# Performance work log

Measured on AMD Instinct MI355X. Metric: run time of the kernel, lower is better.

The kernel has to match this reference:

```python
import jax, jax.numpy as jnp
import numpy as np

N_NODES = 100000
N_EDGES = 3200000
N_GRAPHS = 4096
N_REL = 5
N_BASES = 4
HID = 32


def setup_inputs() -> dict:
    key = jax.random.key(0)
    ks = jax.random.split(key, 32)
    inp = {}
    inp['x'] = jax.random.normal(ks[0], (N_NODES, 4), dtype=jnp.float32)
    inp['edge_index'] = jax.random.randint(ks[1], (2, N_EDGES), 0, N_NODES, dtype=jnp.int64)
    inp['edge_type'] = jax.random.randint(ks[2], (N_EDGES,), 0, N_REL, dtype=jnp.int64)
    inp['user_idx'] = jax.random.randint(ks[3], (N_GRAPHS,), 0, N_NODES, dtype=jnp.int64)
    inp['item_idx'] = jax.random.randint(ks[4], (N_GRAPHS,), 0, N_NODES, dtype=jnp.int64)
    k = 5
    for l in range(4):
        in_c = 4 if l == 0 else HID
        inp[f'basis{l}'] = jax.random.normal(ks[k], (N_BASES, in_c, HID), dtype=jnp.float32) * 0.1; k += 1
        inp[f'comp{l}'] = jax.random.normal(ks[k], (N_REL, N_BASES), dtype=jnp.float32) * 0.5; k += 1
        inp[f'root{l}'] = jax.random.normal(ks[k], (in_c, HID), dtype=jnp.float32) * 0.1; k += 1
        inp[f'bias{l}'] = jax.random.normal(ks[k], (HID,), dtype=jnp.float32) * 0.01; k += 1
    inp['w1'] = jax.random.normal(ks[k], (256, 128), dtype=jnp.float32) * 0.05; k += 1
    inp['b1'] = jnp.zeros((128,), dtype=jnp.float32)
    inp['w2'] = jax.random.normal(ks[k], (128, 1), dtype=jnp.float32) * 0.05; k += 1
    inp['b2'] = jnp.zeros((1,), dtype=jnp.float32)
    return inp


def _rgcn_layer(x, src, key5, inv_cnt, basis, comp, root, bias, n_nodes):
    # mean-aggregate raw source features per (dst, relation): [N, R, in]
    agg = jax.ops.segment_sum(x[src], key5, num_segments=n_nodes * N_REL)
    agg = agg.reshape(n_nodes, N_REL, -1) * inv_cnt
    # basis-decomposed relation weights: W_r = sum_b comp[r,b] * basis[b]
    w = jnp.einsum('rb,bio->rio', comp, basis)  # [R, in, out]
    return jnp.einsum('nri,rio->no', agg, w) + x @ root + bias


def reference(x, edge_index, edge_type, user_idx, item_idx,
              basis0, comp0, root0, bias0,
              basis1, comp1, root1, bias1,
              basis2, comp2, root2, bias2,
              basis3, comp3, root3, bias3,
              w1, b1, w2, b2):
    n_nodes = x.shape[0]
    src, dst = edge_index[0], edge_index[1]
    key5 = dst * N_REL + edge_type  # combined (dst, relation) segment id
    cnt = jax.ops.segment_sum(jnp.ones_like(edge_type, dtype=x.dtype), key5,
                              num_segments=n_nodes * N_REL)
    inv_cnt = (1.0 / jnp.maximum(cnt, 1.0)).reshape(n_nodes, N_REL, 1)
    params = [(basis0, comp0, root0, bias0), (basis1, comp1, root1, bias1),
              (basis2, comp2, root2, bias2), (basis3, comp3, root3, bias3)]
    out = x
    hs = []
    for (basis, comp, root, bias) in params:
        out = jnp.tanh(_rgcn_layer(out, src, key5, inv_cnt, basis, comp, root, bias, n_nodes))
        hs.append(out)
    h = jnp.concatenate(hs, axis=1)            # [N, 128]
    g = jnp.concatenate([h[user_idx], h[item_idx]], axis=1)  # [B, 256]
    z = jax.nn.relu(g @ w1 + b1)
    return (z @ w2 + b2)[:, 0]
```

## Files before the change

kernel.cpp:

```cpp
#include <hip/hip_runtime.h>
#include <hip/hip_bf16.h>
#include <hip/hip_fp16.h>

#define N_NODES 100000
#define N_EDGES 3200000
#define N_GRAPHS 4096
#define N_REL 5
#define N_BASES 4
#define HID 32
#define SEG (N_NODES*N_REL)
#define DUMMY N_NODES

#define NBUCK 392
#define BCAP  10240
#define PBCAP 15360
#define NKEY  1280
#define PTILE 4096

typedef _Float16 half8 __attribute__((ext_vector_type(8)));
typedef float floatx4 __attribute__((ext_vector_type(4)));

static __global__ __launch_bounds__(256) void k_part(const int* __restrict__ ei,
                                                     const int* __restrict__ et,
                                                     int* __restrict__ gcur,
                                                     unsigned long long* __restrict__ part) {
    __shared__ unsigned long long stage[PTILE];
    __shared__ int hist[NBUCK];
    __shared__ int lofs[NBUCK];
    __shared__ int lbase[NBUCK];
    __shared__ int sscan[256];
    int t = threadIdx.x;
    int e0 = blockIdx.x * PTILE;
    int tile_n = N_EDGES - e0; if (tile_n > PTILE) tile_n = PTILE;

    for (int k = t; k < NBUCK; k += 256) hist[k] = 0;
    __syncthreads();
    int src[16], bkt[16], lkey[16];
#pragma unroll
    for (int j = 0; j < 16; j++) {
        int e = e0 + j * 256 + t;
        if (e < N_EDGES) {
            int s = ei[e];
            int d = ei[N_EDGES + e];
            int r = et[e];
            src[j] = s; bkt[j] = d >> 8; lkey[j] = ((d & 255) * 5) + r;
            atomicAdd(&hist[bkt[j]], 1);
        } else bkt[j] = -1;
    }
    __syncthreads();
    int h0 = (2 * t     < NBUCK) ? hist[2 * t]     : 0;
    int h1 = (2 * t + 1 < NBUCK) ? hist[2 * t + 1] : 0;
    int s2 = h0 + h1;
    sscan[t] = s2;
    __syncthreads();
    for (int off = 1; off < 256; off <<= 1) {
        int xv = (t >= off) ? sscan[t - off] : 0;
        __syncthreads();
        sscan[t] += xv;
        __syncthreads();
    }
    int excl = sscan[t] - s2;
    if (2 * t     < NBUCK) lofs[2 * t]     = excl;
    if (2 * t + 1 < NBUCK) lofs[2 * t + 1] = excl + h0;
    for (int k = t; k < NBUCK; k += 256) lbase[k] = atomicAdd(&gcur[k], hist[k]);
    __syncthreads();
    for (int k = t; k < NBUCK; k += 256) hist[k] = 0;
    __syncthreads();
#pragma unroll
    for (int j = 0; j < 16; j++) {
        if (bkt[j] >= 0) {
            int rank = atomicAdd(&hist[bkt[j]], 1);
            stage[lofs[bkt[j]] + rank] =
                ((unsigned long long)(unsigned)((bkt[j] << 16) | lkey[j]) << 32)
                | (unsigned)src[j];
        }
    }
    __syncthreads();
    for (int i = t; i < tile_n; i += 256) {
        unsigned long long u = stage[i];
        unsigned hi = (unsigned)(u >> 32);
        int bb = hi >> 16;
        unsigned long long lk = hi & 0xFFFFu;
        int pos = lbase[bb] + (i - lofs[bb]);
        if (pos < BCAP)
            part[(size_t)bb * BCAP + pos] = (lk << 32) | (u & 0xffffffffULL);
    }
}

static __global__ __launch_bounds__(1024) void k_bsort(const unsigned long long* __restrict__ part,
                                                       const int* __restrict__ gcur,
                                                       int* __restrict__ offs,
                                                       int* __restrict__ cnt,
                                                       int* __restrict__ srcs) {
    __shared__ int lhist[NKEY];
    __shared__ int lscan[NKEY];
    __shared__ int sscan[256];
    __shared__ int lsrc[PBCAP];
    int b = blockIdx.x;
    int t = threadIdx.x;
    int n = gcur[b]; if (n > BCAP) n = BCAP;
    const unsigned long long* reg = part + (size_t)b * BCAP;

    for (int k = t; k < NKEY; k += 1024) lhist[k] = 0;
    __syncthreads();
    for (int i = t; i < n; i += 1024)
        atomicAdd(&lhist[(int)(reg[i] >> 32)], 1);
    __syncthreads();

    int loc[5]; int s5 = 0;
    if (t < 256) {
#pragma unroll
        for (int j = 0; j < 5; j++) { loc[j] = s5; s5 += (lhist[t * 5 + j] + 7) & ~7; }
        sscan[t] = s5;
    }
    __syncthreads();
    for (int off = 1; off < 256; off <<= 1) {
        int x = (t >= off && t < 256) ? sscan[t - off] : 0;
        __syncthreads();
        if (t < 256) sscan[t] += x;
        __syncthreads();
    }
    if (t < 256) {
        int excl = sscan[t] - s5;
#pragma unroll
        for (int j = 0; j < 5; j++) lscan[t * 5 + j] = excl + loc[j];
    }
    __syncthreads();
    int ptot = sscan[255]; if (ptot > PBCAP) ptot = PBCAP;
    int pout = ptot + 16; if (pout > PBCAP) pout = PBCAP;

    int base = b * PBCAP;
    if (t < 256) {
#pragma unroll
        for (int j = 0; j < 5; j++) {
            int k = t * 5 + j;
            int segid = b * NKEY + k;
            if (segid < SEG) {
                cnt[segid]  = lhist[k];
                offs[segid] = base + lscan[k];
            }
        }
    }
    __syncthreads();
    for (int k = t; k < NKEY; k += 1024) lhist[k] = 0;
    for (int i = t; i < pout; i += 1024) lsrc[i] = DUMMY;
    __syncthreads();
    for (int i = t; i < n; i += 1024) {
        unsigned long long u = reg[i];
        int k = (int)(u >> 32);
        int pos = lscan[k] + atomicAdd(&lhist[k], 1);
        if (pos < PBCAP) lsrc[pos] = (int)(u & 0xffffffffULL);
    }
    __syncthreads();
    for (int i = t; i < pout; i += 1024) srcs[base + i] = lsrc[i];
}

static __global__ __launch_bounds__(256) void k_pad(const float* __restrict__ x,
                                                    __half* __restrict__ ht0,
                                                    __half* __restrict__ ht1,
                                                    __half* __restrict__ ht2,
                                                    __half* __restrict__ ht3,
                                                    __half* __restrict__ ht4,
                                                    int* __restrict__ srcs) {
    int tid = blockIdx.x * 256 + threadIdx.x;
    if (tid < (N_NODES + 1) * 32) {
        int nd = tid >> 5, ii = tid & 31;
        float v = (nd < N_NODES && ii < 4) ? x[(nd << 2) + ii] : 0.f;
        ht0[tid] = __float2half(v);
    } else {
        int r = tid - (N_NODES + 1) * 32;
        if (r < 128) {
            __half* hp = (r < 32) ? ht1 : (r < 64) ? ht2 : (r < 96) ? ht3 : ht4;
            hp[N_NODES * 32 + (r & 31)] = __float2half(0.f);
        } else if (r < 144) srcs[NBUCK * PBCAP + (r - 128)] = DUMMY;
    }
}

static __global__ __launch_bounds__(256) void k_wprepB(
    const float* __restrict__ ba0, const float* __restrict__ ro0,
    const float* __restrict__ ba1, const float* __restrict__ ro1,
    const float* __restrict__ ba2, const float* __restrict__ ro2,
    const float* __restrict__ ba3, const float* __restrict__ ro3,
    __half* __restrict__ Wb) {
    int idx = blockIdx.x * 256 + threadIdx.x;
    int j    = idx & 7;
    int lane = (idx >> 3) & 63;
    int tile = (idx >> 9) & 1;
    int ls   = idx >> 10;
    int l    = ls / 5;
    int s    = ls - l * 5;
    const float* basis = (l == 0) ? ba0 : (l == 1) ? ba1 : (l == 2) ? ba2 : ba3;
    const float* root  = (l == 0) ? ro0 : (l == 1) ? ro1 : (l == 2) ? ro2 : ro3;
    int in_c = (l == 0) ? 4 : HID;
    int k = s * 32 + ((lane >> 4) << 3) + j;
    int o = tile * 16 + (lane & 15);
    float v;
    if (k < 128) {
        int b = k >> 5, ii = k & 31;
        v = (ii < in_c) ? basis[(b * in_c + ii) * HID + o] : 0.f;
    } else {
        int ii = k - 128;
        v = (ii < in_c) ? root[ii * HID + o] : 0.f;
    }
    Wb[idx] = __float2half(v);
}

static __global__ __launch_bounds__(256) void k_wprepM(const float* __restrict__ w1,
                                                       __half* __restrict__ Wm) {
    int idx = blockIdx.x * 256 + threadIdx.x;
    int j    = idx & 7;
    int lane = (idx >> 3) & 63;
    int s    = (idx >> 9) & 7;
    int tile = idx >> 12;
    int k = s * 32 + ((lane >> 4) << 3) + j;
    int o = tile * 16 + (lane & 15);
    Wm[idx] = __float2half(w1[k * 128 + o]);
}

static __global__ __launch_bounds__(256, 8) void k_layer(
    const __half2* __restrict__ tab, const int* __restrict__ offs,
    const int* __restrict__ cnt, const int* __restrict__ srcs,
    const float* __restrict__ comp, const __half* __restrict__ Wbl,
    const float* __restrict__ bias, __half* __restrict__ hout) {
    __shared__ __align__(16) __half sAgg16[16 * 176];
    int t = threadIdx.x;
    int wave = t >> 6, q = (t >> 4) & 3, p = t & 15;

    float4 cw0 = *(const float4*)(comp + 0);
    float4 cw1 = *(const float4*)(comp + 4);
    float4 cw2 = *(const float4*)(comp + 8);
    float4 cw3 = *(const float4*)(comp + 12);
    float4 cw4 = *(const float4*)(comp + 16);

    int n = blockIdx.x * 16 + wave * 4 + q;
    int s5 = n * N_REL;
    int oo[6], cc[5];
#pragma unroll
    for (int r = 0; r < 5; r++) { oo[r] = offs[s5 + r]; cc[r] = cnt[s5 + r]; }
    oo[5] = oo[4] + ((cc[4] + 7) & ~7);

    __half2 selfh = tab[n * 16 + p];
    float a0x = 0.f, a0y = 0.f, a1x = 0.f, a1y = 0.f;
    float a2x = 0.f, a2y = 0.f, a3x = 0.f, a3y = 0.f;

#pragma unroll
    for (int r = 0; r < 5; r++) {
        int pR = oo[r], pr = oo[r + 1] - pR;
        const int* sp = srcs + pR;
        int4 e0 = *(const int4*)(sp);
        int4 e1 = *(const int4*)(sp + 4);
        __half2 g0 = tab[e0.x * 16 + p], g1 = tab[e0.y * 16 + p];
        __half2 g2 = tab[e0.z * 16 + p], g3 = tab[e0.w * 16 + p];
        __half2 g4 = tab[e1.x * 16 + p], g5 = tab[e1.y * 16 + p];
        __half2 g6 = tab[e1.z * 16 + p], g7 = tab[e1.w * 16 + p];
        __half2 sb = __hadd2(__hadd2(__hadd2(g0, g1), __hadd2(g2, g3)),
                             __hadd2(__hadd2(g4, g5), __hadd2(g6, g7)));
        float2 bf = __half22float2(sb);
        float Sx = bf.x, Sy = bf.y;
        for (int s8 = 8; s8 < pr; s8 += 8) {
            int4 f0 = *(const int4*)(sp + s8);
            int4 f1 = *(const int4*)(sp + s8 + 4);
            __half2 h0 = tab[f0.x * 16 + p], h1 = tab[f0.y * 16 + p];
            __half2 h2 = tab[f0.z * 16 + p], h3 = tab[f0.w * 16 + p];
            __half2 h4 = tab[f1.x * 16 + p], h5 = tab[f1.y * 16 + p];
            __half2 h6 = tab[f1.z * 16 + p], h7 = tab[f1.w * 16 + p];
            __half2 rb = __hadd2(__hadd2(__hadd2(h0, h1), __hadd2(h2, h3)),
                                 __hadd2(__hadd2(h4, h5), __hadd2(h6, h7)));
            float2 rf = __half22float2(rb);
            Sx += rf.x; Sy += rf.y;
        }
        int cr = cc[r];
        float ic = (cr > 0) ? __builtin_amdgcn_rcpf((float)cr) : 0.f;
        float scx = Sx * ic, scy = Sy * ic;
        float4 cw = (r == 0) ? cw0 : (r == 1) ? cw1 : (r == 2) ? cw2
                  : (r == 3) ? cw3 : cw4;
        a0x += cw.x * scx; a0y += cw.x * scy;
        a1x += cw.y * scx; a1y += cw.y * scy;
        a2x += cw.z * scx; a2y += cw.z * scy;
        a3x += cw.w * scx; a3y += cw.w * scy;
    }
    int nl = wave * 4 + q;
    __half2* row = (__half2*)(sAgg16 + nl * 176);
    row[p]      = __float22half2_rn(make_float2(a0x, a0y));
    row[16 + p] = __float22half2_rn(make_float2(a1x, a1y));
    row[32 + p] = __float22half2_rn(make_float2(a2x, a2y));
    row[48 + p] = __float22half2_rn(make_float2(a3x, a3y));
    row[64 + p] = selfh;
    __syncthreads();

    if (wave < 2) {
        int lane = t & 63;
        floatx4 acc = {0.f, 0.f, 0.f, 0.f};
        const __half* aBase = sAgg16 + (lane & 15) * 176 + ((lane >> 4) << 3);
        const __half* bBase = Wbl + wave * 512 + lane * 8;
#pragma unroll
        for (int s = 0; s < 5; s++) {
            half8 a = *(const half8*)(aBase + s * 32);
            half8 b = *(const half8*)(bBase + s * 1024);
            acc = __builtin_amdgcn_mfma_f32_16x16x32_f16(a, b, acc, 0, 0, 0);
        }
        int o = wave * 16 + (lane & 15);
        float bi = bias[o];
#pragma unroll
        for (int r = 0; r < 4; r++) {
            int node = blockIdx.x * 16 + ((lane >> 4) << 2) + r;
            hout[node * 32 + o] = __float2half(tanhf(acc[r] + bi));
        }
    }
}

static __global__ __launch_bounds__(256) void k_mlp(
    const __half* __restrict__ h1, const __half* __restrict__ h2,
    const __half* __restrict__ h3, const __half* __restrict__ h4,
    const int* __restrict__ uidx, const int* __restrict__ iidx,
    const __half* __restrict__ Wm, const float* __restrict__ b1,
    const float* __restrict__ w2, const float* __restrict__ b2,
    float* __restrict__ out) {
    __shared__ __align__(16) __half sg[16 * 264];
    __shared__ float sacc[4][16];
    int t = threadIdx.x, wave = t >> 6, lane = t & 63;
    int g0 = blockIdx.x * 16;
    int lt = lane >> 4, lp = lane & 15;
    const __half* htab = (lt == 0) ? h1 : (lt == 1) ? h2 : (lt == 2) ? h3 : h4;
#pragma unroll
    for (int gg2 = 0; gg2 < 4; gg2++) {
        int gg = wave * 4 + gg2;
        int g = g0 + gg;
        int u = uidx[g], it = iidx[g];
        __half2* dst = (__half2*)(sg + gg * 264);
        dst[lt * 16 + lp]      = ((const __half2*)(htab + u * 32))[lp];
        dst[64 + lt * 16 + lp] = ((const __half2*)(htab + it * 32))[lp];
    }
    __syncthreads();
    floatx4 acc0 = {0.f, 0.f, 0.f, 0.f}, acc1 = {0.f, 0.f, 0.f, 0.f};
    const __half* aBase = sg + (lane & 15) * 264 + ((lane >> 4) << 3);
    const __half* bB0 = Wm + (wave * 2 + 0) * 4096 + lane * 8;
    const __half* bB1 = Wm + (wave * 2 + 1) * 4096 + lane * 8;
#pragma unroll
    for (int s = 0; s < 8; s++) {
        half8 a  = *(const half8*)(aBase + s * 32);
        half8 f0 = *(const half8*)(bB0 + s * 512);
        half8 f1 = *(const half8*)(bB1 + s * 512);
        acc0 = __builtin_amdgcn_mfma_f32_16x16x32_f16(a, f0, acc0, 0, 0, 0);
        acc1 = __builtin_amdgcn_mfma_f32_16x16x32_f16(a, f1, acc1, 0, 0, 0);
    }
    int o0 = wave * 32 + (lane & 15);
    int o1 = o0 + 16;
    float b10 = b1[o0], b11 = b1[o1], w20 = w2[o0], w21 = w2[o1];
#pragma unroll
    for (int r = 0; r < 4; r++) {
        float z0 = fmaxf(acc0[r] + b10, 0.f);
        float z1 = fmaxf(acc1[r] + b11, 0.f);
        float v = z0 * w20 + z1 * w21;
#pragma unroll
        for (int off = 1; off < 16; off <<= 1) v += __shfl_xor(v, off);
        if ((lane & 15) == 0) sacc[wave][((lane >> 4) << 2) + r] = v;
    }
    __syncthreads();
    if (t < 16)
        out[g0 + t] = sacc[0][t] + sacc[1][t] + sacc[2][t] + sacc[3][t] + b2[0];
}

extern "C" void kernel_launch(void* const* d_in, const int* in_sizes, int n_in,
                              void* d_out, int out_size, void* d_ws, size_t ws_size,
                              hipStream_t stream) {
    const float* x  = (const float*)d_in[0];
    const int*   ei = (const int*)d_in[1];
    const int*   et = (const int*)d_in[2];
    const int*   ui = (const int*)d_in[3];
    const int*   ii = (const int*)d_in[4];
    const float* w1 = (const float*)d_in[21];
    const float* b1 = (const float*)d_in[22];
    const float* w2 = (const float*)d_in[23];
    const float* b2 = (const float*)d_in[24];

    char* ws = (char*)d_ws;
    if (ws_size < 92167680UL) return;
    int*    gcur = (int*)(ws + 0);
    int*    offs = (int*)(ws + 2048);
    int*    cnt  = (int*)(ws + 2002176);
    int*    srcs = (int*)(ws + 4002304);
    __half* Wb   = (__half*)(ws + 28086912);
    __half* Wm   = (__half*)(ws + 28127872);
    __half* ht0  = (__half*)(ws + 28193536);
    __half* ht1  = (__half*)(ws + 34593664);
    __half* ht2  = (__half*)(ws + 40993792);
    __half* ht3  = (__half*)(ws + 47393920);
    __half* ht4  = (__half*)(ws + 53794048);
    unsigned long long* part = (unsigned long long*)(ws + 34593664);

    hipMemsetAsync(gcur, 0, NBUCK * 4, stream);

    k_part<<<(N_EDGES + PTILE - 1) / PTILE, 256, 0, stream>>>(ei, et, gcur, part);
    k_bsort<<<NBUCK, 1024, 0, stream>>>(part, gcur, offs, cnt, srcs);
    k_pad<<<12501, 256, 0, stream>>>(x, ht0, ht1, ht2, ht3, ht4, srcs);
    k_wprepB<<<80, 256, 0, stream>>>(
        (const float*)d_in[5],  (const float*)d_in[7],
        (const float*)d_in[9],  (const float*)d_in[11],
        (const float*)d_in[13], (const float*)d_in[15],
        (const float*)d_in[17], (const float*)d_in[19], Wb);
    k_wprepM<<<128, 256, 0, stream>>>(w1, Wm);

    __half* tabs[5] = {ht0, ht1, ht2, ht3, ht4};
    for (int l = 0; l < 4; l++) {
        const float* comp = (const float*)d_in[6 + 4 * l];
        const float* bias = (const float*)d_in[8 + 4 * l];
        k_layer<<<6250, 256, 0, stream>>>((const __half2*)tabs[l], offs, cnt,
                                          srcs, comp, Wb + l * 5120, bias,
                                          tabs[l + 1]);
    }
    k_mlp<<<256, 256, 0, stream>>>(ht1, ht2, ht3, ht4, ui, ii, Wm, b1, w2, b2,
                                   (float*)d_out);
}
```

Measured before the change: 348.1 us.

## Merge prep kernels into one launch and batch first-chunk gathers across relations

Folds the gcur memset, input padding and weight-packing kernels into a single prep kernel launched before partitioning, and moves the padding-row zeroing into the bucket-sort kernel. In the layer kernel, the first eight source indices for all five relations are loaded up front and their gathers issued together before the tail loops. This is meant to cut launch overhead and expose more outstanding memory requests per thread. It also raises register pressure, and the zeroing inside bsort writes into memory aliased with the partition buffer that other blocks may still be reading.

```diff
diff --git a/kernel.cpp b/kernel.cpp
--- a/kernel.cpp
+++ b/kernel.cpp
@@ -91,7 +91,11 @@
                                                        const int* __restrict__ gcur,
                                                        int* __restrict__ offs,
                                                        int* __restrict__ cnt,
-                                                       int* __restrict__ srcs) {
+                                                       int* __restrict__ srcs,
+                                                       __half* __restrict__ ht1,
+                                                       __half* __restrict__ ht2,
+                                                       __half* __restrict__ ht3,
+                                                       __half* __restrict__ ht4) {
     __shared__ int lhist[NKEY];
     __shared__ int lscan[NKEY];
     __shared__ int sscan[256];
@@ -153,68 +157,68 @@
     }
     __syncthreads();
     for (int i = t; i < pout; i += 1024) srcs[base + i] = lsrc[i];
-}
-
-static __global__ __launch_bounds__(256) void k_pad(const float* __restrict__ x,
-                                                    __half* __restrict__ ht0,
-                                                    __half* __restrict__ ht1,
-                                                    __half* __restrict__ ht2,
-                                                    __half* __restrict__ ht3,
-                                                    __half* __restrict__ ht4,
-                                                    int* __restrict__ srcs) {
-    int tid = blockIdx.x * 256 + threadIdx.x;
-    if (tid < (N_NODES + 1) * 32) {
-        int nd = tid >> 5, ii = tid & 31;
-        float v = (nd < N_NODES && ii < 4) ? x[(nd << 2) + ii] : 0.f;
-        ht0[tid] = __float2half(v);
-    } else {
-        int r = tid - (N_NODES + 1) * 32;
-        if (r < 128) {
-            __half* hp = (r < 32) ? ht1 : (r < 64) ? ht2 : (r < 96) ? ht3 : ht4;
-            hp[N_NODES * 32 + (r & 31)] = __float2half(0.f);
-        } else if (r < 144) srcs[NBUCK * PBCAP + (r - 128)] = DUMMY;
-    }
-}
-
-static __global__ __launch_bounds__(256) void k_wprepB(
+
+    if (b == 0 && t < 128) {
+        __half* hp = (t < 32) ? ht1 : (t < 64) ? ht2 : (t < 96) ? ht3 : ht4;
+        hp[N_NODES * 32 + (t & 31)] = __float2half(0.f);
+    }
+}
+
+static __global__ __launch_bounds__(256) void k_prep(
+    const float* __restrict__ x, __half* __restrict__ ht0,
+    int* __restrict__ srcs, int* __restrict__ gcur,
     const float* __restrict__ ba0, const float* __restrict__ ro0,
     const float* __restrict__ ba1, const float* __restrict__ ro1,
     const float* __restrict__ ba2, const float* __restrict__ ro2,
     const float* __restrict__ ba3, const float* __restrict__ ro3,
-    __half* __restrict__ Wb) {
-    int idx = blockIdx.x * 256 + threadIdx.x;
-    int j    = idx & 7;
-    int lane = (idx >> 3) & 63;
-    int tile = (idx >> 9) & 1;
-    int ls   = idx >> 10;
-    int l    = ls / 5;
-    int s    = ls - l * 5;
-    const float* basis = (l == 0) ? ba0 : (l == 1) ? ba1 : (l == 2) ? ba2 : ba3;
-    const float* root  = (l == 0) ? ro0 : (l == 1) ? ro1 : (l == 2) ? ro2 : ro3;
-    int in_c = (l == 0) ? 4 : HID;
-    int k = s * 32 + ((lane >> 4) << 3) + j;
-    int o = tile * 16 + (lane & 15);
-    float v;
-    if (k < 128) {
-        int b = k >> 5, ii = k & 31;
-        v = (ii < in_c) ? basis[(b * in_c + ii) * HID + o] : 0.f;
+    const float* __restrict__ w1, __half* __restrict__ Wb,
+    __half* __restrict__ Wm) {
+    int blk = blockIdx.x;
+    int t = threadIdx.x;
+    if (blk < 12501) {
+        int tid = blk * 256 + t;
+        if (tid < (N_NODES + 1) * 32) {
+            int nd = tid >> 5, ii = tid & 31;
+            float v = (nd < N_NODES && ii < 4) ? x[(nd << 2) + ii] : 0.f;
+            ht0[tid] = __float2half(v);
+        } else {
+            int r = tid - (N_NODES + 1) * 32;
+            if (r < 16) srcs[NBUCK * PBCAP + r] = DUMMY;
+        }
+    } else if (blk < 12581) {
+        int idx = (blk - 12501) * 256 + t;
+        int j    = idx & 7;
+        int lane = (idx >> 3) & 63;
+        int tile = (idx >> 9) & 1;
+        int ls   = idx >> 10;
+        int l    = ls / 5;
+        int s    = ls - l * 5;
+        const float* basis = (l == 0) ? ba0 : (l == 1) ? ba1 : (l == 2) ? ba2 : ba3;
+        const float* root  = (l == 0) ? ro0 : (l == 1) ? ro1 : (l == 2) ? ro2 : ro3;
+        int in_c = (l == 0) ? 4 : HID;
+        int k = s * 32 + ((lane >> 4) << 3) + j;
+        int o = tile * 16 + (lane & 15);
+        float v;
+        if (k < 128) {
+            int b = k >> 5, ii = k & 31;
+            v = (ii < in_c) ? basis[(b * in_c + ii) * HID + o] : 0.f;
+        } else {
+            int ii = k - 128;
+            v = (ii < in_c) ? root[ii * HID + o] : 0.f;
+        }
+        Wb[idx] = __float2half(v);
+    } else if (blk < 12709) {
+        int idx = (blk - 12581) * 256 + t;
+        int j    = idx & 7;
+        int lane = (idx >> 3) & 63;
+        int s    = (idx >> 9) & 7;
+        int tile = idx >> 12;
+        int k = s * 32 + ((lane >> 4) << 3) + j;
+        int o = tile * 16 + (lane & 15);
+        Wm[idx] = __float2half(w1[k * 128 + o]);
     } else {
-        int ii = k - 128;
-        v = (ii < in_c) ? root[ii * HID + o] : 0.f;
-    }
-    Wb[idx] = __float2half(v);
-}
-
-static __global__ __launch_bounds__(256) void k_wprepM(const float* __restrict__ w1,
-                                                       __half* __restrict__ Wm) {
-    int idx = blockIdx.x * 256 + threadIdx.x;
-    int j    = idx & 7;
-    int lane = (idx >> 3) & 63;
-    int s    = (idx >> 9) & 7;
-    int tile = idx >> 12;
-    int k = s * 32 + ((lane >> 4) << 3) + j;
-    int o = tile * 16 + (lane & 15);
-    Wm[idx] = __float2half(w1[k * 128 + o]);
+        for (int k = t; k < NBUCK; k += 256) gcur[k] = 0;
+    }
 }
 
 static __global__ __launch_bounds__(256, 8) void k_layer(
@@ -240,23 +244,30 @@
     oo[5] = oo[4] + ((cc[4] + 7) & ~7);
 
     __half2 selfh = tab[n * 16 + p];
-    float a0x = 0.f, a0y = 0.f, a1x = 0.f, a1y = 0.f;
-    float a2x = 0.f, a2y = 0.f, a3x = 0.f, a3y = 0.f;
-
+
+    int4 e0[5], e1[5];
 #pragma unroll
     for (int r = 0; r < 5; r++) {
-        int pR = oo[r], pr = oo[r + 1] - pR;
-        const int* sp = srcs + pR;
-        int4 e0 = *(const int4*)(sp);
-        int4 e1 = *(const int4*)(sp + 4);
-        __half2 g0 = tab[e0.x * 16 + p], g1 = tab[e0.y * 16 + p];
-        __half2 g2 = tab[e0.z * 16 + p], g3 = tab[e0.w * 16 + p];
-        __half2 g4 = tab[e1.x * 16 + p], g5 = tab[e1.y * 16 + p];
-        __half2 g6 = tab[e1.z * 16 + p], g7 = tab[e1.w * 16 + p];
+        const int4* sp4 = (const int4*)(srcs + oo[r]);
+        e0[r] = sp4[0];
+        e1[r] = sp4[1];
+    }
+    float Sx[5], Sy[5];
+#pragma unroll
+    for (int r = 0; r < 5; r++) {
+        __half2 g0 = tab[e0[r].x * 16 + p], g1 = tab[e0[r].y * 16 + p];
+        __half2 g2 = tab[e0[r].z * 16 + p], g3 = tab[e0[r].w * 16 + p];
+        __half2 g4 = tab[e1[r].x * 16 + p], g5 = tab[e1[r].y * 16 + p];
+        __half2 g6 = tab[e1[r].z * 16 + p], g7 = tab[e1[r].w * 16 + p];
         __half2 sb = __hadd2(__hadd2(__hadd2(g0, g1), __hadd2(g2, g3)),
                              __hadd2(__hadd2(g4, g5), __hadd2(g6, g7)));
         float2 bf = __half22float2(sb);
-        float Sx = bf.x, Sy = bf.y;
+        Sx[r] = bf.x; Sy[r] = bf.y;
+    }
+#pragma unroll
+    for (int r = 0; r < 5; r++) {
+        int pr = oo[r + 1] - oo[r];
+        const int* sp = srcs + oo[r];
         for (int s8 = 8; s8 < pr; s8 += 8) {
             int4 f0 = *(const int4*)(sp + s8);
             int4 f1 = *(const int4*)(sp + s8 + 4);
@@ -267,11 +278,16 @@
             __half2 rb = __hadd2(__hadd2(__hadd2(h0, h1), __hadd2(h2, h3)),
                                  __hadd2(__hadd2(h4, h5), __hadd2(h6, h7)));
             float2 rf = __half22float2(rb);
-            Sx += rf.x; Sy += rf.y;
-        }
+            Sx[r] += rf.x; Sy[r] += rf.y;
+        }
+    }
+    float a0x = 0.f, a0y = 0.f, a1x = 0.f, a1y = 0.f;
+    float a2x = 0.f, a2y = 0.f, a3x = 0.f, a3y = 0.f;
+#pragma unroll
+    for (int r = 0; r < 5; r++) {
         int cr = cc[r];
         float ic = (cr > 0) ? __builtin_amdgcn_rcpf((float)cr) : 0.f;
-        float scx = Sx * ic, scy = Sy * ic;
+        float scx = Sx[r] * ic, scy = Sy[r] * ic;
         float4 cw = (r == 0) ? cw0 : (r == 1) ? cw1 : (r == 2) ? cw2
                   : (r == 3) ? cw3 : cw4;
         a0x += cw.x * scx; a0y += cw.x * scy;
@@ -389,17 +405,14 @@
     __half* ht4  = (__half*)(ws + 53794048);
     unsigned long long* part = (unsigned long long*)(ws + 34593664);
 
-    hipMemsetAsync(gcur, 0, NBUCK * 4, stream);
-
-    k_part<<<(N_EDGES + PTILE - 1) / PTILE, 256, 0, stream>>>(ei, et, gcur, part);
-    k_bsort<<<NBUCK, 1024, 0, stream>>>(part, gcur, offs, cnt, srcs);
-    k_pad<<<12501, 256, 0, stream>>>(x, ht0, ht1, ht2, ht3, ht4, srcs);
-    k_wprepB<<<80, 256, 0, stream>>>(
+    k_prep<<<12710, 256, 0, stream>>>(x, ht0, srcs, gcur,
         (const float*)d_in[5],  (const float*)d_in[7],
         (const float*)d_in[9],  (const float*)d_in[11],
         (const float*)d_in[13], (const float*)d_in[15],
-        (const float*)d_in[17], (const float*)d_in[19], Wb);
-    k_wprepM<<<128, 256, 0, stream>>>(w1, Wm);
+        (const float*)d_in[17], (const float*)d_in[19], w1, Wb, Wm);
+    k_part<<<(N_EDGES + PTILE - 1) / PTILE, 256, 0, stream>>>(ei, et, gcur, part);
+    k_bsort<<<NBUCK, 1024, 0, stream>>>(part, gcur, offs, cnt, srcs,
+                                        ht1, ht2, ht3, ht4);
 
     __half* tabs[5] = {ht0, ht1, ht2, ht3, ht4};
     for (int l = 0; l < 4; l++) {
```

New measurement: 724.1 us. 108% more time.
